# Performance work log

Hardware: AMD Instinct MI355X
Metric: run time of the kernel (lower is better)

## Reference

```python
import jax, jax.numpy as jnp
import numpy as np

N = 50000
E = 800000
IN_CH = 64
HID = 128
K1 = 64
K2 = 16
THR = 1.0 / (K1 - 1)
EPS_LN = 1e-5


def setup_inputs() -> dict:
    key = jax.random.key(0)
    ks = jax.random.split(key, 10)
    def w(k, shape):
        return jax.random.normal(k, shape, jnp.float32) / np.sqrt(shape[0]).astype(np.float32)
    return {
        "x": jax.random.normal(ks[0], (N, IN_CH), jnp.float32),
        "edge_index": jax.random.randint(ks[1], (2, E), 0, N),
        "W1_rel": w(ks[2], (IN_CH, HID)),
        "b1_rel": jnp.zeros((HID,), jnp.float32),
        "W1_root": w(ks[3], (IN_CH, HID)),
        "Wp1": w(ks[4], (HID, K1)),
        "bp1": jnp.zeros((K1,), jnp.float32),
        "ln1_w": jnp.ones((K1,), jnp.float32),
        "ln1_b": jnp.zeros((K1,), jnp.float32),
        "W2_rel": w(ks[5], (HID, HID)),
        "b2_rel": jnp.zeros((HID,), jnp.float32),
        "W2_root": w(ks[6], (HID, HID)),
        "Wp2": w(ks[7], (HID, K2)),
        "bp2": jnp.zeros((K2,), jnp.float32),
        "ln2_w": jnp.ones((K2,), jnp.float32),
        "ln2_b": jnp.zeros((K2,), jnp.float32),
    }


def _layer_norm(x, w, b):
    m = x.mean(-1, keepdims=True)
    v = ((x - m) ** 2).mean(-1, keepdims=True)
    return (x - m) / jnp.sqrt(v + EPS_LN) * w + b


def _mincut_core(x, s, A_s, deg):
    # s already softmaxed. A_s[i] = sum_j A[i,j] s[j]; deg[i] = sum_j A[i,j].
    k = s.shape[1]
    pooled_x = s.T @ x                       # [k, F]
    pooled_adj = s.T @ A_s                   # [k, k]
    mincut_num = jnp.trace(pooled_adj)
    mincut_den = jnp.trace(s.T @ (deg[:, None] * s)) + 1e-10
    mincut_loss = -mincut_num / mincut_den
    sT_s = s.T @ s
    nrm = jnp.linalg.norm(sT_s)
    eye = jnp.eye(k, dtype=s.dtype)
    ortho_loss = jnp.linalg.norm(sT_s / (nrm + 1e-10) - eye / np.sqrt(k).astype(np.float32))
    adj = pooled_adj * (1.0 - eye)           # zero diagonal
    d_sqrt = jnp.sqrt(adj.sum(1))[:, None]
    inv = 1.0 / (d_sqrt + 1e-15)
    adj_norm = adj * inv * inv.T
    return pooled_x, adj_norm, mincut_loss, ortho_loss


def _forward(x, edge_index, W1_rel, b1_rel, W1_root, Wp1, bp1, ln1_w, ln1_b,
             W2_rel, b2_rel, W2_root, Wp2, bp2, ln2_w, ln2_b):
    n = x.shape[0]
    src, dst = edge_index[0], edge_index[1]
    # GraphConv 1: sum-aggregate source features at target, then linear + root
    agg1 = jax.ops.segment_sum(x[src], dst, num_segments=n)
    x1 = jax.nn.relu(agg1 @ W1_rel + b1_rel + x @ W1_root)
    s1 = _layer_norm(x1 @ Wp1 + bp1, ln1_w, ln1_b)
    s1_soft = jax.nn.softmax(s1, axis=-1)
    # sparse mincut pool 1 (edge list, unit weights): A_s[row] += s[col]
    A_s1 = jax.ops.segment_sum(s1_soft[src], src * 0 + src, num_segments=n) if False else jax.ops.segment_sum(s1_soft[dst], src, num_segments=n)
    deg1 = jax.ops.segment_sum(jnp.ones((E,), x.dtype), src, num_segments=n)
    x_pool1, adj1, mc1, o1 = _mincut_core(x1, s1_soft, A_s1, deg1)
    # threshold -> binary coarse adjacency (replaces torch nonzero edge list)
    A1 = jnp.where(adj1 > THR, 1.0, 0.0).astype(x.dtype)    # [K1, K1]
    # GraphConv 2 on dense binary A1 (edges (r,c): message x[r] -> node c)
    agg2 = A1.T @ x_pool1
    x2 = jax.nn.relu(agg2 @ W2_rel + b2_rel + x_pool1 @ W2_root)
    s2 = _layer_norm(x2 @ Wp2 + bp2, ln2_w, ln2_b)
    s2_soft = jax.nn.softmax(s2, axis=-1)
    A_s2 = A1 @ s2_soft
    deg2 = A1.sum(1)
    _, adj2, mc2, o2 = _mincut_core(x2, s2_soft, A_s2, deg2)
    return (mc1, o1, mc2, o2, s1, A1, s2, adj2)


def reference(x, edge_index, W1_rel, b1_rel, W1_root, Wp1, bp1, ln1_w, ln1_b,
              W2_rel, b2_rel, W2_root, Wp2, bp2, ln2_w, ln2_b):
    return _forward(x, edge_index, W1_rel, b1_rel, W1_root, Wp1, bp1, ln1_w, ln1_b,
                    W2_rel, b2_rel, W2_root, Wp2, bp2, ln2_w, ln2_b)
```

## Files before the change

kernel.cpp:

```cpp
#include <hip/hip_runtime.h>

#define NN 50000
#define EE 800000
#define NT32 1563
#define NTILE 3125
#define NSB 196
#define MAXSLAB 768

#define OUT_S1 4
#define OUT_A1 (4 + NN * 64)
#define OUT_S2 (OUT_A1 + 64 * 64)
#define OUT_ADJ2 (OUT_S2 + 64 * 16)

__device__ __forceinline__ float block_sum256(float v, float* red) {
  v += __shfl_xor(v, 32); v += __shfl_xor(v, 16); v += __shfl_xor(v, 8);
  v += __shfl_xor(v, 4);  v += __shfl_xor(v, 2);  v += __shfl_xor(v, 1);
  __syncthreads();
  if ((threadIdx.x & 63) == 0) red[threadIdx.x >> 6] = v;
  __syncthreads();
  return red[0] + red[1] + red[2] + red[3];
}

__device__ __forceinline__ float4 gather_rows64(
    const float* __restrict__ rows, const int* __restrict__ csr,
    int off, int c, int l, int g) {
  float4 a0 = make_float4(0.f, 0.f, 0.f, 0.f);
  float4 a1 = a0, a2 = a0, a3 = a0;
  int bb = 0;
  for (; bb + 16 <= c; bb += 16) {
    int myid = csr[off + bb + l];
    #pragma unroll
    for (int j = 0; j < 16; j += 4) {
      int s0 = __shfl(myid, g + j + 0, 64);
      int s1 = __shfl(myid, g + j + 1, 64);
      int s2 = __shfl(myid, g + j + 2, 64);
      int s3 = __shfl(myid, g + j + 3, 64);
      const float4 v0 = *(const float4*)&rows[(size_t)s0 * 64 + l * 4];
      const float4 v1 = *(const float4*)&rows[(size_t)s1 * 64 + l * 4];
      const float4 v2 = *(const float4*)&rows[(size_t)s2 * 64 + l * 4];
      const float4 v3 = *(const float4*)&rows[(size_t)s3 * 64 + l * 4];
      a0.x += v0.x; a0.y += v0.y; a0.z += v0.z; a0.w += v0.w;
      a1.x += v1.x; a1.y += v1.y; a1.z += v1.z; a1.w += v1.w;
      a2.x += v2.x; a2.y += v2.y; a2.z += v2.z; a2.w += v2.w;
      a3.x += v3.x; a3.y += v3.y; a3.z += v3.z; a3.w += v3.w;
    }
  }
  int m = c - bb;
  if (m > 0) {
    int myid = (l < m) ? csr[off + bb + l] : 0;
    int j = 0;
    for (; j + 2 <= m; j += 2) {
      int s0 = __shfl(myid, g + j + 0, 64);
      int s1 = __shfl(myid, g + j + 1, 64);
      const float4 v0 = *(const float4*)&rows[(size_t)s0 * 64 + l * 4];
      const float4 v1 = *(const float4*)&rows[(size_t)s1 * 64 + l * 4];
      a0.x += v0.x; a0.y += v0.y; a0.z += v0.z; a0.w += v0.w;
      a1.x += v1.x; a1.y += v1.y; a1.z += v1.z; a1.w += v1.w;
    }
    if (j < m) {
      int s0 = __shfl(myid, g + j, 64);
      const float4 v0 = *(const float4*)&rows[(size_t)s0 * 64 + l * 4];
      a2.x += v0.x; a2.y += v0.y; a2.z += v0.z; a2.w += v0.w;
    }
  }
  a0.x += a1.x; a0.y += a1.y; a0.z += a1.z; a0.w += a1.w;
  a2.x += a3.x; a2.y += a3.y; a2.z += a3.z; a2.w += a3.w;
  a0.x += a2.x; a0.y += a2.y; a0.z += a2.z; a0.w += a2.w;
  return a0;
}

__global__ __launch_bounds__(256) void k_hist(
    const int* __restrict__ ei, int* __restrict__ cnt_dst, int* __restrict__ deg_src) {
  int e = blockIdx.x * 256 + threadIdx.x;
  int s = ei[e], d = ei[EE + e];
  atomicAdd(&cnt_dst[d], 1);
  atomicAdd(&deg_src[s], 1);
}

__global__ __launch_bounds__(256) void k_scan1(
    const int* __restrict__ cnt, int* __restrict__ cursor, int* __restrict__ bsum) {
  __shared__ int sh[256];
  int t = threadIdx.x;
  int idx = blockIdx.x * 256 + t;
  int v = (idx < NN) ? cnt[idx] : 0;
  sh[t] = v;
  __syncthreads();
  for (int o = 1; o < 256; o <<= 1) {
    int u = (t >= o) ? sh[t - o] : 0;
    __syncthreads();
    sh[t] += u;
    __syncthreads();
  }
  if (idx < NN) cursor[idx] = sh[t] - v;
  if (t == 255) bsum[blockIdx.x] = sh[255];
}

__global__ __launch_bounds__(256) void k_scan2(int* __restrict__ bsum) {
  __shared__ int sh[256];
  int t = threadIdx.x;
  int v = (t < NSB) ? bsum[t] : 0;
  sh[t] = v;
  __syncthreads();
  for (int o = 1; o < 256; o <<= 1) {
    int u = (t >= o) ? sh[t - o] : 0;
    __syncthreads();
    sh[t] += u;
    __syncthreads();
  }
  if (t < NSB) bsum[t] = sh[t] - v;
}

__global__ __launch_bounds__(256) void k_scan3(
    int* __restrict__ cursor, const int* __restrict__ bsum) {
  int idx = blockIdx.x * 256 + threadIdx.x;
  if (idx < NN) cursor[idx] += bsum[blockIdx.x];
}

__global__ __launch_bounds__(256) void k_fill(
    const int* __restrict__ ei, int* __restrict__ cursor, int* __restrict__ csr) {
  int e = blockIdx.x * 256 + threadIdx.x;
  int s = ei[e], d = ei[EE + e];
  int pos = atomicAdd(&cursor[d], 1);
  csr[pos] = s;
}

__global__ __launch_bounds__(256, 4) void k_fused1(
    const float* __restrict__ x, const int* __restrict__ csr,
    const int* __restrict__ cur_end, const int* __restrict__ cnt,
    const int* __restrict__ deg_src,
    const float* __restrict__ W1rel, const float* __restrict__ b1,
    const float* __restrict__ W1root,
    const float* __restrict__ Wp1, const float* __restrict__ bp1,
    const float* __restrict__ lnw, const float* __restrict__ lnb,
    float* __restrict__ x1, float* __restrict__ s1_out,
    float* __restrict__ s1s, float* __restrict__ den) {
  __shared__ float smem[4224];
  __shared__ float dred[32];
  float* agg_t = smem;
  float* x_t   = smem + 2048;
  float* x1_t  = smem;
  int t = threadIdx.x;
  int base = blockIdx.x * 32;

  {
    int n16 = t >> 4, l = t & 15;
    #pragma unroll
    for (int half = 0; half < 2; ++half) {
      int n = n16 + half * 16;
      int node = base + n;
      if (node < NN) {
        *(float4*)&x_t[n * 64 + l * 4] = *(const float4*)&x[(size_t)node * 64 + l * 4];
        int c = cnt[node];
        int off = cur_end[node] - c;
        float4 acc = gather_rows64(x, csr, off, c, l, t & 48);
        *(float4*)&agg_t[n * 64 + l * 4] = acc;
      } else {
        float4 z = make_float4(0.f, 0.f, 0.f, 0.f);
        *(float4*)&x_t[n * 64 + l * 4] = z;
        *(float4*)&agg_t[n * 64 + l * 4] = z;
      }
    }
  }
  __syncthreads();

  int rg = t >> 5, cg = t & 31;
  int r0 = rg * 4;
  int c4 = cg * 4;
  float4 r0v, r1v, r2v, r3v;
  {
    float4 acc0 = *(const float4*)&b1[c4];
    float4 acc1 = acc0, acc2 = acc0, acc3 = acc0;
    #pragma unroll 4
    for (int k = 0; k < 64; ++k) {
      const float4 w1 = *(const float4*)&W1rel[k * 128 + c4];
      const float4 w2 = *(const float4*)&W1root[k * 128 + c4];
      float a0 = agg_t[(r0 + 0) * 64 + k], e0 = x_t[(r0 + 0) * 64 + k];
      float a1 = agg_t[(r0 + 1) * 64 + k], e1 = x_t[(r0 + 1) * 64 + k];
      float a2 = agg_t[(r0 + 2) * 64 + k], e2 = x_t[(r0 + 2) * 64 + k];
      float a3 = agg_t[(r0 + 3) * 64 + k], e3 = x_t[(r0 + 3) * 64 + k];
      acc0.x += a0 * w1.x + e0 * w2.x; acc0.y += a0 * w1.y + e0 * w2.y;
      acc0.z += a0 * w1.z + e0 * w2.z; acc0.w += a0 * w1.w + e0 * w2.w;
      acc1.x += a1 * w1.x + e1 * w2.x; acc1.y += a1 * w1.y + e1 * w2.y;
      acc1.z += a1 * w1.z + e1 * w2.z; acc1.w += a1 * w1.w + e1 * w2.w;
      acc2.x += a2 * w1.x + e2 * w2.x; acc2.y += a2 * w1.y + e2 * w2.y;
      acc2.z += a2 * w1.z + e2 * w2.z; acc2.w += a2 * w1.w + e2 * w2.w;
      acc3.x += a3 * w1.x + e3 * w2.x; acc3.y += a3 * w1.y + e3 * w2.y;
      acc3.z += a3 * w1.z + e3 * w2.z; acc3.w += a3 * w1.w + e3 * w2.w;
    }
    r0v.x = fmaxf(acc0.x, 0.f); r0v.y = fmaxf(acc0.y, 0.f);
    r0v.z = fmaxf(acc0.z, 0.f); r0v.w = fmaxf(acc0.w, 0.f);
    r1v.x = fmaxf(acc1.x, 0.f); r1v.y = fmaxf(acc1.y, 0.f);
    r1v.z = fmaxf(acc1.z, 0.f); r1v.w = fmaxf(acc1.w, 0.f);
    r2v.x = fmaxf(acc2.x, 0.f); r2v.y = fmaxf(acc2.y, 0.f);
    r2v.z = fmaxf(acc2.z, 0.f); r2v.w = fmaxf(acc2.w, 0.f);
    r3v.x = fmaxf(acc3.x, 0.f); r3v.y = fmaxf(acc3.y, 0.f);
    r3v.z = fmaxf(acc3.z, 0.f); r3v.w = fmaxf(acc3.w, 0.f);
    if (base + r0 + 3 < NN) {
      *(float4*)&x1[(size_t)(base + r0 + 0) * 128 + c4] = r0v;
      *(float4*)&x1[(size_t)(base + r0 + 1) * 128 + c4] = r1v;
      *(float4*)&x1[(size_t)(base + r0 + 2) * 128 + c4] = r2v;
      *(float4*)&x1[(size_t)(base + r0 + 3) * 128 + c4] = r3v;
    } else {
      if (base + r0 + 0 < NN) *(float4*)&x1[(size_t)(base + r0 + 0) * 128 + c4] = r0v;
      if (base + r0 + 1 < NN) *(float4*)&x1[(size_t)(base + r0 + 1) * 128 + c4] = r1v;
      if (base + r0 + 2 < NN) *(float4*)&x1[(size_t)(base + r0 + 2) * 128 + c4] = r2v;
    }
  }
  __syncthreads();
  *(float4*)&x1_t[(r0 + 0) * 132 + c4] = r0v;
  *(float4*)&x1_t[(r0 + 1) * 132 + c4] = r1v;
  *(float4*)&x1_t[(r0 + 2) * 132 + c4] = r2v;
  *(float4*)&x1_t[(r0 + 3) * 132 + c4] = r3v;
  __syncthreads();

  {
    int c2 = cg * 2;
    const float2 b0 = *(const float2*)&bp1[c2];
    float2 acc0 = b0, acc1 = b0, acc2 = b0, acc3 = b0;
    #pragma unroll 4
    for (int k0 = 0; k0 < 128; k0 += 4) {
      const float2 w0 = *(const float2*)&Wp1[(k0 + 0) * 64 + c2];
      const float2 w1 = *(const float2*)&Wp1[(k0 + 1) * 64 + c2];
      const float2 w2 = *(const float2*)&Wp1[(k0 + 2) * 64 + c2];
      const float2 w3 = *(const float2*)&Wp1[(k0 + 3) * 64 + c2];
      const float4 x0 = *(const float4*)&x1_t[(r0 + 0) * 132 + k0];
      const float4 x1v = *(const float4*)&x1_t[(r0 + 1) * 132 + k0];
      const float4 x2v = *(const float4*)&x1_t[(r0 + 2) * 132 + k0];
      const float4 x3v = *(const float4*)&x1_t[(r0 + 3) * 132 + k0];
      acc0.x += x0.x * w0.x + x0.y * w1.x + x0.z * w2.x + x0.w * w3.x;
      acc0.y += x0.x * w0.y + x0.y * w1.y + x0.z * w2.y + x0.w * w3.y;
      acc1.x += x1v.x * w0.x + x1v.y * w1.x + x1v.z * w2.x + x1v.w * w3.x;
      acc1.y += x1v.x * w0.y + x1v.y * w1.y + x1v.z * w2.y + x1v.w * w3.y;
      acc2.x += x2v.x * w0.x + x2v.y * w1.x + x2v.z * w2.x + x2v.w * w3.x;
      acc2.y += x2v.x * w0.y + x2v.y * w1.y + x2v.z * w2.y + x2v.w * w3.y;
      acc3.x += x3v.x * w0.x + x3v.y * w1.x + x3v.z * w2.x + x3v.w * w3.x;
      acc3.y += x3v.x * w0.y + x3v.y * w1.y + x3v.z * w2.y + x3v.w * w3.y;
    }
    const float2 lw = *(const float2*)&lnw[c2];
    const float2 lb = *(const float2*)&lnb[c2];
    float2 accs[4] = {acc0, acc1, acc2, acc3};
    #pragma unroll
    for (int i = 0; i < 4; ++i) {
      int r = r0 + i;
      int row = base + r;
      float ax = accs[i].x, ay = accs[i].y;
      float m = ax + ay;
      m += __shfl_xor(m, 1); m += __shfl_xor(m, 2); m += __shfl_xor(m, 4);
      m += __shfl_xor(m, 8); m += __shfl_xor(m, 16);
      m *= (1.0f / 64.0f);
      float dx = ax - m, dy = ay - m;
      float v = dx * dx + dy * dy;
      v += __shfl_xor(v, 1); v += __shfl_xor(v, 2); v += __shfl_xor(v, 4);
      v += __shfl_xor(v, 8); v += __shfl_xor(v, 16);
      v *= (1.0f / 64.0f);
      float rstd = rsqrtf(v + 1e-5f);
      float lnx = dx * rstd * lw.x + lb.x;
      float lny = dy * rstd * lw.y + lb.y;
      float mx = fmaxf(lnx, lny);
      mx = fmaxf(mx, __shfl_xor(mx, 1)); mx = fmaxf(mx, __shfl_xor(mx, 2));
      mx = fmaxf(mx, __shfl_xor(mx, 4)); mx = fmaxf(mx, __shfl_xor(mx, 8));
      mx = fmaxf(mx, __shfl_xor(mx, 16));
      float ex = expf(lnx - mx), ey = expf(lny - mx);
      float se = ex + ey;
      se += __shfl_xor(se, 1); se += __shfl_xor(se, 2); se += __shfl_xor(se, 4);
      se += __shfl_xor(se, 8); se += __shfl_xor(se, 16);
      float inv = 1.0f / se;
      ex *= inv; ey *= inv;
      float ss = ex * ex + ey * ey;
      ss += __shfl_xor(ss, 1); ss += __shfl_xor(ss, 2); ss += __shfl_xor(ss, 4);
      ss += __shfl_xor(ss, 8); ss += __shfl_xor(ss, 16);
      if (row < NN) {
        *(float2*)&s1_out[(size_t)row * 64 + c2] = make_float2(lnx, lny);
        *(float2*)&s1s[(size_t)row * 64 + c2] = make_float2(ex, ey);
        if (cg == 0) dred[r] = ss * (float)deg_src[row];
      } else if (cg == 0) {
        dred[r] = 0.f;
      }
    }
  }
  __syncthreads();
  if (t == 0) {
    float s = 0.f;
    #pragma unroll
    for (int i = 0; i < 32; ++i) s += dred[i];
    atomicAdd(den, s);
  }
}

__global__ __launch_bounds__(256) void k_pooled_all(
    const float* __restrict__ s1s, const float* __restrict__ x1,
    const int* __restrict__ csr, const int* __restrict__ cur_end,
    const int* __restrict__ cnt, float* __restrict__ part) {
  __shared__ float s_t[1024];
  __shared__ float g_t[1024];
  __shared__ float x_t[2048];
  int t = threadIdx.x;
  int kg = t >> 5;
  int cg = t & 31;
  int c1 = cg * 4;
  int cc = (cg & 15) * 4;
  bool is_padj = (cg < 16);
  float a1[8][4], a2[8][4];
  #pragma unroll
  for (int j = 0; j < 8; ++j)
    #pragma unroll
    for (int q = 0; q < 4; ++q) { a1[j][q] = 0.f; a2[j][q] = 0.f; }

  for (int tile = blockIdx.x; tile < NTILE; tile += gridDim.x) {
    size_t base = (size_t)tile * 16;
    __syncthreads();
    *(float4*)&s_t[t * 4] = *(const float4*)&s1s[base * 64 + t * 4];
    *(float4*)&x_t[t * 8] = *(const float4*)&x1[base * 128 + t * 8];
    *(float4*)&x_t[t * 8 + 4] = *(const float4*)&x1[base * 128 + t * 8 + 4];
    {
      int n16 = t >> 4, l = t & 15;
      int node = (int)base + n16;
      int c = cnt[node];
      int off = cur_end[node] - c;
      float4 acc = gather_rows64(s1s, csr, off, c, l, t & 48);
      *(float4*)&g_t[n16 * 64 + l * 4] = acc;
    }
    __syncthreads();
    #pragma unroll 2
    for (int r = 0; r < 16; ++r) {
      const float4 xv = *(const float4*)&x_t[r * 128 + c1];
      const float4 sv = *(const float4*)&s_t[r * 64 + cc];
      const float4 k0 = *(const float4*)&s_t[r * 64 + kg * 8];
      const float4 k1 = *(const float4*)&s_t[r * 64 + kg * 8 + 4];
      const float4 g0 = *(const float4*)&g_t[r * 64 + kg * 8];
      const float4 g1 = *(const float4*)&g_t[r * 64 + kg * 8 + 4];
      float sk[8] = {k0.x, k0.y, k0.z, k0.w, k1.x, k1.y, k1.z, k1.w};
      float gk[8] = {g0.x, g0.y, g0.z, g0.w, g1.x, g1.y, g1.z, g1.w};
      #pragma unroll
      for (int j = 0; j < 8; ++j) {
        float m2 = is_padj ? gk[j] : sk[j];
        a1[j][0] += sk[j] * xv.x; a1[j][1] += sk[j] * xv.y;
        a1[j][2] += sk[j] * xv.z; a1[j][3] += sk[j] * xv.w;
        a2[j][0] += m2 * sv.x; a2[j][1] += m2 * sv.y;
        a2[j][2] += m2 * sv.z; a2[j][3] += m2 * sv.w;
      }
    }
  }
  float* slab = part + (size_t)blockIdx.x * 16384;
  float* o2base = slab + (is_padj ? 8192 : 12288);
  #pragma unroll
  for (int j = 0; j < 8; ++j) {
    int k = kg * 8 + j;
    *(float4*)&slab[k * 128 + c1] = make_float4(a1[j][0], a1[j][1], a1[j][2], a1[j][3]);
    *(float4*)&o2base[k * 64 + cc] = make_float4(a2[j][0], a2[j][1], a2[j][2], a2[j][3]);
  }
}

__global__ __launch_bounds__(256) void k_reduce1(
    const float* __restrict__ part, int nslab, int chunk,
    float* __restrict__ part2) {
  int ib = blockIdx.x & 15;
  int bs = blockIdx.x >> 4;
  int i4 = ib * 256 + threadIdx.x;
  int b0 = bs * chunk;
  int b1 = b0 + chunk; if (b1 > nslab) b1 = nslab;
  float4 acc = make_float4(0.f, 0.f, 0.f, 0.f);
  for (int b = b0; b < b1; ++b) {
    const float4 v = *(const float4*)&part[(size_t)b * 16384 + (size_t)i4 * 4];
    acc.x += v.x; acc.y += v.y; acc.z += v.z; acc.w += v.w;
  }
  *(float4*)&part2[(size_t)bs * 16384 + (size_t)i4 * 4] = acc;
}

__global__ __launch_bounds__(256) void k_reduce2(
    const float* __restrict__ part2, float* __restrict__ dst) {
  int i = blockIdx.x * 256 + threadIdx.x;
  float acc = 0.f;
  #pragma unroll
  for (int b = 0; b < 32; ++b) acc += part2[b * 16384 + i];
  dst[i] = acc;
}

__global__ __launch_bounds__(256) void k_p2a(
    const float* __restrict__ padj_g, const float* __restrict__ sts_g,
    const float* __restrict__ den_g, const float* __restrict__ px_g,
    float* __restrict__ out, float* __restrict__ A1f, float* __restrict__ agg2) {
  __shared__ float padj[4096];
  __shared__ float A1s[4096];
  __shared__ float invs[64];
  __shared__ float red[4];
  int t = threadIdx.x;
  for (int i = t; i < 4096; i += 256) padj[i] = padj_g[i];
  __syncthreads();
  float num = (t < 64) ? padj[t * 64 + t] : 0.f;
  num = block_sum256(num, red);
  float n2 = 0.f;
  for (int i = t; i < 4096; i += 256) { float v = sts_g[i]; n2 += v * v; }
  n2 = block_sum256(n2, red);
  float nrm = sqrtf(n2);
  float oacc = 0.f;
  for (int i = t; i < 4096; i += 256) {
    float v = sts_g[i] / (nrm + 1e-10f);
    if ((i >> 6) == (i & 63)) v -= 0.125f;
    oacc += v * v;
  }
  oacc = block_sum256(oacc, red);
  if (t == 0) {
    out[0] = -num / (den_g[0] + 1e-10f);
    out[1] = sqrtf(oacc);
  }
  if (t < 64) {
    float rs = 0.f;
    for (int j = 0; j < 64; ++j)
      if (j != t) rs += padj[t * 64 + j];
    invs[t] = 1.0f / (sqrtf(rs) + 1e-15f);
  }
  __syncthreads();
  const float THRv = 1.0f / 63.0f;
  for (int i = t; i < 4096; i += 256) {
    int r = i >> 6, c = i & 63;
    float a = (r == c) ? 0.f : padj[i] * invs[r] * invs[c];
    float b = (a > THRv) ? 1.0f : 0.0f;
    out[OUT_A1 + i] = b;
    A1f[i] = b;
    A1s[i] = b;
  }
  __syncthreads();
  int j = t >> 2, q = t & 3;
  float acc[32];
  #pragma unroll
  for (int c = 0; c < 32; ++c) acc[c] = 0.f;
  for (int i = 0; i < 64; ++i) {
    float a = A1s[i * 64 + j];
    const float* pxr = px_g + i * 128 + q * 32;
    #pragma unroll
    for (int c = 0; c < 32; ++c) acc[c] += a * pxr[c];
  }
  #pragma unroll
  for (int c = 0; c < 32; ++c) agg2[j * 128 + q * 32 + c] = acc[c];
}

__global__ __launch_bounds__(128) void k_x2(
    const float* __restrict__ agg2, const float* __restrict__ px,
    const float* __restrict__ W2rel, const float* __restrict__ b2,
    const float* __restrict__ W2root, float* __restrict__ x2) {
  int row = blockIdx.x, col = threadIdx.x;
  const float* ar = agg2 + row * 128;
  const float* xr = px + row * 128;
  float acc = b2[col];
  #pragma unroll 4
  for (int k = 0; k < 128; ++k)
    acc += ar[k] * W2rel[k * 128 + col] + xr[k] * W2root[k * 128 + col];
  x2[row * 128 + col] = fmaxf(acc, 0.f);
}

__global__ __launch_bounds__(256) void k_p2c(
    const float* __restrict__ x2g, const float* __restrict__ Wp2,
    const float* __restrict__ bp2, const float* __restrict__ lnw,
    const float* __restrict__ lnb, const float* __restrict__ A1f,
    float* __restrict__ out) {
  __shared__ float A1s[4096];
  __shared__ float s2lin[1024];
  __shared__ float s2s[1024];
  __shared__ float As2[1024];
  __shared__ float deg2[64];
  __shared__ float padj2[256];
  __shared__ float sts2[256];
  __shared__ float inv2[16];
  __shared__ float red[4];
  int t = threadIdx.x;
  for (int i = t; i < 4096; i += 256) A1s[i] = A1f[i];
  for (int it = 0; it < 4; ++it) {
    int idx = t + it * 256;
    int r = idx >> 4, c = idx & 15;
    float acc = bp2[c];
    const float* xr = x2g + r * 128;
    #pragma unroll 8
    for (int k = 0; k < 128; ++k) acc += xr[k] * Wp2[k * 16 + c];
    s2lin[idx] = acc;
  }
  __syncthreads();
  if (t < 64) {
    float m = 0.f;
    #pragma unroll
    for (int c = 0; c < 16; ++c) m += s2lin[t * 16 + c];
    m *= (1.0f / 16.0f);
    float v = 0.f;
    #pragma unroll
    for (int c = 0; c < 16; ++c) { float d = s2lin[t * 16 + c] - m; v += d * d; }
    v *= (1.0f / 16.0f);
    float rstd = rsqrtf(v + 1e-5f);
    float mx = -1e30f;
    float lnv[16];
    #pragma unroll
    for (int c = 0; c < 16; ++c) {
      lnv[c] = (s2lin[t * 16 + c] - m) * rstd * lnw[c] + lnb[c];
      out[OUT_S2 + t * 16 + c] = lnv[c];
      mx = fmaxf(mx, lnv[c]);
    }
    float se = 0.f;
    #pragma unroll
    for (int c = 0; c < 16; ++c) { float e = expf(lnv[c] - mx); s2s[t * 16 + c] = e; se += e; }
    float inv = 1.0f / se;
    #pragma unroll
    for (int c = 0; c < 16; ++c) s2s[t * 16 + c] *= inv;
    float dg = 0.f;
    for (int j = 0; j < 64; ++j) dg += A1s[t * 64 + j];
    deg2[t] = dg;
  }
  __syncthreads();
  for (int it = 0; it < 4; ++it) {
    int idx = t + it * 256;
    int i = idx >> 4, c = idx & 15;
    float acc = 0.f;
    for (int j = 0; j < 64; ++j) acc += A1s[i * 64 + j] * s2s[j * 16 + c];
    As2[idx] = acc;
  }
  __syncthreads();
  {
    int a = t >> 4, b = t & 15;
    float acc = 0.f, accs = 0.f;
    for (int i = 0; i < 64; ++i) {
      float sa = s2s[i * 16 + a];
      acc += sa * As2[i * 16 + b];
      accs += sa * s2s[i * 16 + b];
    }
    padj2[t] = acc;
    sts2[t] = accs;
  }
  __syncthreads();
  float num2 = (t < 16) ? padj2[t * 17] : 0.f;
  num2 = block_sum256(num2, red);
  float dpart = 0.f;
  if (t < 64) {
    float ss = 0.f;
    #pragma unroll
    for (int c = 0; c < 16; ++c) ss += s2s[t * 16 + c] * s2s[t * 16 + c];
    dpart = deg2[t] * ss;
  }
  float den2 = block_sum256(dpart, red);
  float n2 = sts2[t] * sts2[t];
  n2 = block_sum256(n2, red);
  float nrm2 = sqrtf(n2);
  float ov;
  {
    float v = sts2[t] / (nrm2 + 1e-10f);
    if ((t >> 4) == (t & 15)) v -= 0.25f;
    ov = v * v;
  }
  ov = block_sum256(ov, red);
  if (t == 0) {
    out[2] = -num2 / (den2 + 1e-10f);
    out[3] = sqrtf(ov);
  }
  if (t < 16) {
    float rs = 0.f;
    #pragma unroll
    for (int b = 0; b < 16; ++b)
      if (b != t) rs += padj2[t * 16 + b];
    inv2[t] = 1.0f / (sqrtf(rs) + 1e-15f);
  }
  __syncthreads();
  {
    int a = t >> 4, b = t & 15;
    float v = (a == b) ? 0.f : padj2[t] * inv2[a] * inv2[b];
    out[OUT_ADJ2 + t] = v;
  }
}

extern "C" void kernel_launch(void* const* d_in, const int* in_sizes, int n_in,
                              void* d_out, int out_size, void* d_ws, size_t ws_size,
                              hipStream_t stream) {
  const float* x      = (const float*)d_in[0];
  const int*   ei     = (const int*)d_in[1];
  const float* W1_rel = (const float*)d_in[2];
  const float* b1_rel = (const float*)d_in[3];
  const float* W1_root= (const float*)d_in[4];
  const float* Wp1    = (const float*)d_in[5];
  const float* bp1    = (const float*)d_in[6];
  const float* ln1w   = (const float*)d_in[7];
  const float* ln1b   = (const float*)d_in[8];
  const float* W2_rel = (const float*)d_in[9];
  const float* b2_rel = (const float*)d_in[10];
  const float* W2_root= (const float*)d_in[11];
  const float* Wp2    = (const float*)d_in[12];
  const float* bp2    = (const float*)d_in[13];
  const float* ln2w   = (const float*)d_in[14];
  const float* ln2b   = (const float*)d_in[15];
  float* out = (float*)d_out;

  int* cnt_dst = (int*)d_ws;
  int* deg_src = cnt_dst + NN;
  int* cursor  = deg_src + NN;
  int* bsum    = cursor + NN;
  int* csr     = bsum + 256;
  float* x1    = (float*)(csr + EE);
  float* s1s   = x1 + (size_t)NN * 128;
  float* dst   = s1s + (size_t)NN * 64;
  float* px    = dst;
  float* padj  = dst + 8192;
  float* sts   = dst + 12288;
  float* den   = dst + 16384;
  float* A1f   = den + 4;
  float* agg2  = A1f + 4096;
  float* x2    = agg2 + 8192;
  float* part2 = x2 + 8192;
  float* part  = part2 + 32 * 16384;

  size_t used_floats = (size_t)(part - (float*)d_ws);
  size_t avail = ws_size / 4 - used_floats;
  int nslab = (int)(avail / 16384);
  if (nslab > MAXSLAB) nslab = MAXSLAB;
  if (nslab < 1) nslab = 1;
  int chunk = (nslab + 31) / 32;

  hipMemsetAsync(cnt_dst, 0, 2 * NN * sizeof(int), stream);
  hipMemsetAsync(den, 0, sizeof(float), stream);

  k_hist<<<EE / 256, 256, 0, stream>>>(ei, cnt_dst, deg_src);
  k_scan1<<<NSB, 256, 0, stream>>>(cnt_dst, cursor, bsum);
  k_scan2<<<1, 256, 0, stream>>>(bsum);
  k_scan3<<<NSB, 256, 0, stream>>>(cursor, bsum);
  k_fill<<<EE / 256, 256, 0, stream>>>(ei, cursor, csr);
  k_fused1<<<NT32, 256, 0, stream>>>(x, csr, cursor, cnt_dst, deg_src,
                                     W1_rel, b1_rel, W1_root, Wp1, bp1,
                                     ln1w, ln1b, x1, out + OUT_S1, s1s, den);
  k_pooled_all<<<nslab, 256, 0, stream>>>(s1s, x1, csr, cursor, cnt_dst, part);
  k_reduce1<<<512, 256, 0, stream>>>(part, nslab, chunk, part2);
  k_reduce2<<<64, 256, 0, stream>>>(part2, dst);
  k_p2a<<<1, 256, 0, stream>>>(padj, sts, den, px, out, A1f, agg2);
  k_x2<<<64, 128, 0, stream>>>(agg2, px, W2_rel, b2_rel, W2_root, x2);
  k_p2c<<<1, 256, 0, stream>>>(x2, Wp2, bp2, ln2w, ln2b, A1f, out);
}
```

Baseline: 425.0 us.

## Compute mincut denominator from gathered softmax rows and drop source-degree histogram

```diff
diff --git a/kernel.cpp b/kernel.cpp
--- a/kernel.cpp
+++ b/kernel.cpp
@@ -5,7 +5,7 @@
 #define NT32 1563
 #define NTILE 3125
 #define NSB 196
-#define MAXSLAB 768
+#define MAXSLAB 1024
 
 #define OUT_S1 4
 #define OUT_A1 (4 + NN * 64)
@@ -69,12 +69,66 @@
   return a0;
 }
 
+__device__ __forceinline__ float4 gather_rows64_sq(
+    const float* __restrict__ rows, const int* __restrict__ csr,
+    int off, int c, int l, int g, float& dsq) {
+  float4 a0 = make_float4(0.f, 0.f, 0.f, 0.f);
+  float4 a1 = a0, a2 = a0, a3 = a0;
+  int bb = 0;
+  for (; bb + 16 <= c; bb += 16) {
+    int myid = csr[off + bb + l];
+    #pragma unroll
+    for (int j = 0; j < 16; j += 4) {
+      int s0 = __shfl(myid, g + j + 0, 64);
+      int s1 = __shfl(myid, g + j + 1, 64);
+      int s2 = __shfl(myid, g + j + 2, 64);
+      int s3 = __shfl(myid, g + j + 3, 64);
+      const float4 v0 = *(const float4*)&rows[(size_t)s0 * 64 + l * 4];
+      const float4 v1 = *(const float4*)&rows[(size_t)s1 * 64 + l * 4];
+      const float4 v2 = *(const float4*)&rows[(size_t)s2 * 64 + l * 4];
+      const float4 v3 = *(const float4*)&rows[(size_t)s3 * 64 + l * 4];
+      a0.x += v0.x; a0.y += v0.y; a0.z += v0.z; a0.w += v0.w;
+      a1.x += v1.x; a1.y += v1.y; a1.z += v1.z; a1.w += v1.w;
+      a2.x += v2.x; a2.y += v2.y; a2.z += v2.z; a2.w += v2.w;
+      a3.x += v3.x; a3.y += v3.y; a3.z += v3.z; a3.w += v3.w;
+      dsq += v0.x * v0.x + v0.y * v0.y + v0.z * v0.z + v0.w * v0.w;
+      dsq += v1.x * v1.x + v1.y * v1.y + v1.z * v1.z + v1.w * v1.w;
+      dsq += v2.x * v2.x + v2.y * v2.y + v2.z * v2.z + v2.w * v2.w;
+      dsq += v3.x * v3.x + v3.y * v3.y + v3.z * v3.z + v3.w * v3.w;
+    }
+  }
+  int m = c - bb;
+  if (m > 0) {
+    int myid = (l < m) ? csr[off + bb + l] : 0;
+    int j = 0;
+    for (; j + 2 <= m; j += 2) {
+      int s0 = __shfl(myid, g + j + 0, 64);
+      int s1 = __shfl(myid, g + j + 1, 64);
+      const float4 v0 = *(const float4*)&rows[(size_t)s0 * 64 + l * 4];
+      const float4 v1 = *(const float4*)&rows[(size_t)s1 * 64 + l * 4];
+      a0.x += v0.x; a0.y += v0.y; a0.z += v0.z; a0.w += v0.w;
+      a1.x += v1.x; a1.y += v1.y; a1.z += v1.z; a1.w += v1.w;
+      dsq += v0.x * v0.x + v0.y * v0.y + v0.z * v0.z + v0.w * v0.w;
+      dsq += v1.x * v1.x + v1.y * v1.y + v1.z * v1.z + v1.w * v1.w;
+    }
+    if (j < m) {
+      int s0 = __shfl(myid, g + j, 64);
+      const float4 v0 = *(const float4*)&rows[(size_t)s0 * 64 + l * 4];
+      a2.x += v0.x; a2.y += v0.y; a2.z += v0.z; a2.w += v0.w;
+      dsq += v0.x * v0.x + v0.y * v0.y + v0.z * v0.z + v0.w * v0.w;
+    }
+  }
+  a0.x += a1.x; a0.y += a1.y; a0.z += a1.z; a0.w += a1.w;
+  a2.x += a3.x; a2.y += a3.y; a2.z += a3.z; a2.w += a3.w;
+  a0.x += a2.x; a0.y += a2.y; a0.z += a2.z; a0.w += a2.w;
+  return a0;
+}
+
 __global__ __launch_bounds__(256) void k_hist(
-    const int* __restrict__ ei, int* __restrict__ cnt_dst, int* __restrict__ deg_src) {
+    const int* __restrict__ ei, int* __restrict__ cnt_dst) {
   int e = blockIdx.x * 256 + threadIdx.x;
-  int s = ei[e], d = ei[EE + e];
+  int d = ei[EE + e];
   atomicAdd(&cnt_dst[d], 1);
-  atomicAdd(&deg_src[s], 1);
 }
 
 __global__ __launch_bounds__(256) void k_scan1(
@@ -110,32 +164,26 @@
   if (t < NSB) bsum[t] = sh[t] - v;
 }
 
-__global__ __launch_bounds__(256) void k_scan3(
-    int* __restrict__ cursor, const int* __restrict__ bsum) {
-  int idx = blockIdx.x * 256 + threadIdx.x;
-  if (idx < NN) cursor[idx] += bsum[blockIdx.x];
-}
-
 __global__ __launch_bounds__(256) void k_fill(
-    const int* __restrict__ ei, int* __restrict__ cursor, int* __restrict__ csr) {
+    const int* __restrict__ ei, int* __restrict__ cursor,
+    const int* __restrict__ bsum, int* __restrict__ csr) {
   int e = blockIdx.x * 256 + threadIdx.x;
   int s = ei[e], d = ei[EE + e];
-  int pos = atomicAdd(&cursor[d], 1);
+  int pos = atomicAdd(&cursor[d], 1) + bsum[d >> 8];
   csr[pos] = s;
 }
 
 __global__ __launch_bounds__(256, 4) void k_fused1(
     const float* __restrict__ x, const int* __restrict__ csr,
     const int* __restrict__ cur_end, const int* __restrict__ cnt,
-    const int* __restrict__ deg_src,
+    const int* __restrict__ bsum,
     const float* __restrict__ W1rel, const float* __restrict__ b1,
     const float* __restrict__ W1root,
     const float* __restrict__ Wp1, const float* __restrict__ bp1,
     const float* __restrict__ lnw, const float* __restrict__ lnb,
     float* __restrict__ x1, float* __restrict__ s1_out,
-    float* __restrict__ s1s, float* __restrict__ den) {
+    float* __restrict__ s1s) {
   __shared__ float smem[4224];
-  __shared__ float dred[32];
   float* agg_t = smem;
   float* x_t   = smem + 2048;
   float* x1_t  = smem;
@@ -151,7 +199,7 @@
       if (node < NN) {
         *(float4*)&x_t[n * 64 + l * 4] = *(const float4*)&x[(size_t)node * 64 + l * 4];
         int c = cnt[node];
-        int off = cur_end[node] - c;
+        int off = cur_end[node] - c + bsum[node >> 8];
         float4 acc = gather_rows64(x, csr, off, c, l, t & 48);
         *(float4*)&agg_t[n * 64 + l * 4] = acc;
       } else {
@@ -241,8 +289,7 @@
     float2 accs[4] = {acc0, acc1, acc2, acc3};
     #pragma unroll
     for (int i = 0; i < 4; ++i) {
-      int r = r0 + i;
-      int row = base + r;
+      int row = base + r0 + i;
       float ax = accs[i].x, ay = accs[i].y;
       float m = ax + ay;
       m += __shfl_xor(m, 1); m += __shfl_xor(m, 2); m += __shfl_xor(m, 4);
@@ -266,34 +313,23 @@
       se += __shfl_xor(se, 8); se += __shfl_xor(se, 16);
       float inv = 1.0f / se;
       ex *= inv; ey *= inv;
-      float ss = ex * ex + ey * ey;
-      ss += __shfl_xor(ss, 1); ss += __shfl_xor(ss, 2); ss += __shfl_xor(ss, 4);
-      ss += __shfl_xor(ss, 8); ss += __shfl_xor(ss, 16);
       if (row < NN) {
         *(float2*)&s1_out[(size_t)row * 64 + c2] = make_float2(lnx, lny);
         *(float2*)&s1s[(size_t)row * 64 + c2] = make_float2(ex, ey);
-        if (cg == 0) dred[r] = ss * (float)deg_src[row];
-      } else if (cg == 0) {
-        dred[r] = 0.f;
       }
     }
   }
-  __syncthreads();
-  if (t == 0) {
-    float s = 0.f;
-    #pragma unroll
-    for (int i = 0; i < 32; ++i) s += dred[i];
-    atomicAdd(den, s);
-  }
-}
-
-__global__ __launch_bounds__(256) void k_pooled_all(
+}
+
+__global__ __launch_bounds__(256, 4) void k_pooled_all(
     const float* __restrict__ s1s, const float* __restrict__ x1,
     const int* __restrict__ csr, const int* __restrict__ cur_end,
-    const int* __restrict__ cnt, float* __restrict__ part) {
+    const int* __restrict__ cnt, const int* __restrict__ bsum,
+    float* __restrict__ part, float* __restrict__ den) {
   __shared__ float s_t[1024];
   __shared__ float g_t[1024];
   __shared__ float x_t[2048];
+  __shared__ float red[4];
   int t = threadIdx.x;
   int kg = t >> 5;
   int cg = t & 31;
@@ -301,6 +337,7 @@
   int cc = (cg & 15) * 4;
   bool is_padj = (cg < 16);
   float a1[8][4], a2[8][4];
+  float dsq = 0.f;
   #pragma unroll
   for (int j = 0; j < 8; ++j)
     #pragma unroll
@@ -316,8 +353,8 @@
       int n16 = t >> 4, l = t & 15;
       int node = (int)base + n16;
       int c = cnt[node];
-      int off = cur_end[node] - c;
-      float4 acc = gather_rows64(s1s, csr, off, c, l, t & 48);
+      int off = cur_end[node] - c + bsum[node >> 8];
+      float4 acc = gather_rows64_sq(s1s, csr, off, c, l, t & 48, dsq);
       *(float4*)&g_t[n16 * 64 + l * 4] = acc;
     }
     __syncthreads();
@@ -349,6 +386,8 @@
     *(float4*)&slab[k * 128 + c1] = make_float4(a1[j][0], a1[j][1], a1[j][2], a1[j][3]);
     *(float4*)&o2base[k * 64 + cc] = make_float4(a2[j][0], a2[j][1], a2[j][2], a2[j][3]);
   }
+  float dtot = block_sum256(dsq, red);
+  if (t == 0) atomicAdd(den, dtot);
 }
 
 __global__ __launch_bounds__(256) void k_reduce1(
@@ -585,8 +624,7 @@
   float* out = (float*)d_out;
 
   int* cnt_dst = (int*)d_ws;
-  int* deg_src = cnt_dst + NN;
-  int* cursor  = deg_src + NN;
+  int* cursor  = cnt_dst + NN;
   int* bsum    = cursor + NN;
   int* csr     = bsum + 256;
   float* x1    = (float*)(csr + EE);
@@ -609,18 +647,18 @@
   if (nslab < 1) nslab = 1;
   int chunk = (nslab + 31) / 32;
 
-  hipMemsetAsync(cnt_dst, 0, 2 * NN * sizeof(int), stream);
+  hipMemsetAsync(cnt_dst, 0, NN * sizeof(int), stream);
   hipMemsetAsync(den, 0, sizeof(float), stream);
 
-  k_hist<<<EE / 256, 256, 0, stream>>>(ei, cnt_dst, deg_src);
+  k_hist<<<EE / 256, 256, 0, stream>>>(ei, cnt_dst);
   k_scan1<<<NSB, 256, 0, stream>>>(cnt_dst, cursor, bsum);
   k_scan2<<<1, 256, 0, stream>>>(bsum);
-  k_scan3<<<NSB, 256, 0, stream>>>(cursor, bsum);
-  k_fill<<<EE / 256, 256, 0, stream>>>(ei, cursor, csr);
-  k_fused1<<<NT32, 256, 0, stream>>>(x, csr, cursor, cnt_dst, deg_src,
+  k_fill<<<EE / 256, 256, 0, stream>>>(ei, cursor, bsum, csr);
+  k_fused1<<<NT32, 256, 0, stream>>>(x, csr, cursor, cnt_dst, bsum,
                                      W1_rel, b1_rel, W1_root, Wp1, bp1,
-                                     ln1w, ln1b, x1, out + OUT_S1, s1s, den);
-  k_pooled_all<<<nslab, 256, 0, stream>>>(s1s, x1, csr, cursor, cnt_dst, part);
+                                     ln1w, ln1b, x1, out + OUT_S1, s1s);
+  k_pooled_all<<<nslab, 256, 0, stream>>>(s1s, x1, csr, cursor, cnt_dst, bsum,
+                                          part, den);
   k_reduce1<<<512, 256, 0, stream>>>(part, nslab, chunk, part2);
   k_reduce2<<<64, 256, 0, stream>>>(part2, dst);
   k_p2a<<<1, 256, 0, stream>>>(padj, sts, den, px, out, A1f, agg2);
```

New measurement: 406.4 us. 4.4% less time.
